# Kernel tuning notes

Measured on AMD Instinct MI355X. Metric: run time of the kernel, lower is better.

The kernel has to match this reference:

```python
import jax, jax.numpy as jnp
import numpy as np

# LLaMA-style decoder config (shrunken for reference): L layers, hidden D, H heads,
# SwiGLU width F, vocab V, LoRA rank R.
B, S, D, H, F, V, L, R = 2, 512, 1024, 16, 4096, 32000, 2, 16
DH = D // H
LORA_ALPHA = 32.0
EPS = 1e-5
ROPE_THETA = 10000.0


def setup_inputs() -> dict:
    key = jax.random.key(0)
    ks = iter(jax.random.split(key, 40))
    def n(shape, std=0.02):
        return jax.random.normal(next(ks), shape, jnp.float32) * std
    return {
        "input_ids": jax.random.randint(next(ks), (B, S), 0, V),
        "attention_mask": jnp.ones((B, S), jnp.int32),
        "embed": n((V, D)),
        "ln1": jnp.ones((L, D), jnp.float32),
        "ln2": jnp.ones((L, D), jnp.float32),
        "wq": n((L, D, D)), "aq": n((L, D, R)), "bq": n((L, R, D), 0.01),
        "wk": n((L, D, D)), "ak": n((L, D, R)), "bk": n((L, R, D), 0.01),
        "wv": n((L, D, D)), "av": n((L, D, R)), "bv": n((L, R, D), 0.01),
        "wo": n((L, D, D)), "ao": n((L, D, R)), "bo": n((L, R, D), 0.01),
        "wg": n((L, D, F)), "ag": n((L, D, R)), "bg": n((L, R, F), 0.01),
        "wu": n((L, D, F)), "au": n((L, D, R)), "bu": n((L, R, F), 0.01),
        "wd": n((L, F, D)), "ad": n((L, F, R)), "bd": n((L, R, D), 0.01),
        "final_ln": jnp.ones((D,), jnp.float32),
        "lm_head_w": n((D, V)),
        "value_w": n((D, 1)),
        "value_b": jnp.zeros((1,), jnp.float32),
    }


def _rmsnorm(x, w):
    return x * jax.lax.rsqrt(jnp.mean(x * x, axis=-1, keepdims=True) + EPS) * w


def _lin_lora(x, w, a, b):
    # base matmul + low-rank LoRA update scaled by alpha/r (dropout=eval/off)
    return x @ w + ((x @ a) @ b) * (LORA_ALPHA / R)


def _rope_cache(seq_len):
    half = DH // 2
    inv = 1.0 / (ROPE_THETA ** (jnp.arange(half, dtype=jnp.float32) / half))
    ang = jnp.arange(seq_len, dtype=jnp.float32)[:, None] * inv  # [S, half]
    ang = jnp.concatenate([ang, ang], axis=-1)                   # [S, DH]
    return jnp.cos(ang), jnp.sin(ang)


def _apply_rope(x, cos, sin):  # x: [B,S,H,DH]
    h = DH // 2
    rot = jnp.concatenate([-x[..., h:], x[..., :h]], axis=-1)
    return x * cos[None, :, None, :] + rot * sin[None, :, None, :]


def reference(input_ids, attention_mask, embed, ln1, ln2,
              wq, aq, bq, wk, ak, bk, wv, av, bv, wo, ao, bo,
              wg, ag, bg, wu, au, bu, wd, ad, bd,
              final_ln, lm_head_w, value_w, value_b):
    h = embed[input_ids]  # [B,S,D]
    cos, sin = _rope_cache(S)
    causal = jnp.tril(jnp.ones((S, S), bool))
    keep = causal[None, None, :, :] & (attention_mask[:, None, None, :] > 0)
    bias = jnp.where(keep, 0.0, -1e9)  # [B,1,S,S]
    scale = 1.0 / jnp.sqrt(jnp.float32(DH))

    for i in range(L):
        # --- self-attention block ---
        x = _rmsnorm(h, ln1[i])
        q = _lin_lora(x, wq[i], aq[i], bq[i]).reshape(B, S, H, DH)
        k = _lin_lora(x, wk[i], ak[i], bk[i]).reshape(B, S, H, DH)
        v = _lin_lora(x, wv[i], av[i], bv[i]).reshape(B, S, H, DH)
        q = _apply_rope(q, cos, sin)
        k = _apply_rope(k, cos, sin)
        scores = jnp.einsum("bqhd,bkhd->bhqk", q, k) * scale + bias
        attn = jax.nn.softmax(scores, axis=-1)
        o = jnp.einsum("bhqk,bkhd->bqhd", attn, v).reshape(B, S, D)
        h = h + _lin_lora(o, wo[i], ao[i], bo[i])
        # --- SwiGLU MLP block ---
        x = _rmsnorm(h, ln2[i])
        g = jax.nn.silu(_lin_lora(x, wg[i], ag[i], bg[i]))
        u = _lin_lora(x, wu[i], au[i], bu[i])
        h = h + _lin_lora(g * u, wd[i], ad[i], bd[i])

    h = _rmsnorm(h, final_ln)          # HF hidden_states[-1] is post final norm
    logits = h @ lm_head_w             # [B,S,V]
    values = (h @ value_w)[..., 0] + value_b[0]  # [B,S] (squeeze(-1))
    return logits, values
```

## Files before the change

kernel.cpp:

```cpp
#include <hip/hip_runtime.h>
#include <math.h>

constexpr int B = 2, S = 512, D = 1024, H = 16, F = 4096, V = 32000, L = 2, R = 16, DH = 64;
constexpr int BS = B * S;
constexpr float LORA_SCALE = 2.0f;
constexpr float EPS = 1e-5f;
constexpr int RS_QKV = 3 * D;
constexpr int RS_GU  = 2 * F;

typedef __attribute__((ext_vector_type(8))) __bf16 bf16x8;
typedef __attribute__((ext_vector_type(4))) float f32x4;

__device__ __forceinline__ unsigned short f2bf(float f) {
  unsigned u = __builtin_bit_cast(unsigned, f);
  unsigned r = (u + 0x7FFFu + ((u >> 16) & 1u)) >> 16;
  return (unsigned short)r;
}
__device__ __forceinline__ float bf2f(unsigned short us) {
  return __builtin_bit_cast(float, (unsigned)us << 16);
}
__device__ __forceinline__ void load_lds16(const void* g, void* l) {
  __builtin_amdgcn_global_load_lds((const __attribute__((address_space(1))) void*)g,
                                   (__attribute__((address_space(3))) void*)l, 16, 0, 0);
}

struct Ptr3 { const float* p[3]; };

__global__ void rope_cache_kernel(float* __restrict__ cosb, float* __restrict__ sinb) {
  int s = blockIdx.x, j = threadIdx.x;
  float inv = __expf(-(float)j * (9.210340371976184f / 32.0f));
  float ang = (float)s * inv;
  float c = cosf(ang), sn = sinf(ang);
  cosb[s * DH + j] = c;  cosb[s * DH + j + 32] = c;
  sinb[s * DH + j] = sn; sinb[s * DH + j + 32] = sn;
}

__global__ void embed_kernel(const int* __restrict__ ids, const float* __restrict__ emb,
                             float* __restrict__ h) {
  int row = blockIdx.x, t = threadIdx.x;
  int id = ids[row];
  ((float4*)(h + (size_t)row * D))[t] = ((const float4*)(emb + (size_t)id * D))[t];
}

__global__ void rmsnorm_bf16_kernel(const float* __restrict__ x, const float* __restrict__ w,
                                    unsigned short* __restrict__ y) {
  int row = blockIdx.x, t = threadIdx.x;
  float4 xv = ((const float4*)(x + (size_t)row * D))[t];
  float ss = xv.x * xv.x + xv.y * xv.y + xv.z * xv.z + xv.w * xv.w;
  __shared__ float red[256];
  red[t] = ss; __syncthreads();
  for (int s2 = 128; s2; s2 >>= 1) { if (t < s2) red[t] += red[t + s2]; __syncthreads(); }
  float rinv = rsqrtf(red[0] * (1.0f / D) + EPS);
  float4 wv = ((const float4*)w)[t];
  ushort4 o;
  o.x = f2bf(xv.x * rinv * wv.x); o.y = f2bf(xv.y * rinv * wv.y);
  o.z = f2bf(xv.z * rinv * wv.z); o.w = f2bf(xv.w * rinv * wv.w);
  ((ushort4*)(y + (size_t)row * D))[t] = o;
}

template <int NA>
__global__ void rms_lora_kernel(const float* __restrict__ hp, const float* __restrict__ w,
                                Ptr3 ap, unsigned short* __restrict__ xbf,
                                unsigned short* __restrict__ t2e) {
  int row = blockIdx.x, t = threadIdx.x;
  __shared__ float xs[D];
  __shared__ float red[256];
  float4 xv = ((const float4*)(hp + (size_t)row * D))[t];
  float ss = xv.x * xv.x + xv.y * xv.y + xv.z * xv.z + xv.w * xv.w;
  red[t] = ss; __syncthreads();
  for (int s2 = 128; s2; s2 >>= 1) { if (t < s2) red[t] += red[t + s2]; __syncthreads(); }
  float rinv = rsqrtf(red[0] * (1.0f / D) + EPS);
  float4 wv = ((const float4*)w)[t];
  float4 nx;
  nx.x = xv.x * rinv * wv.x; nx.y = xv.y * rinv * wv.y;
  nx.z = xv.z * rinv * wv.z; nx.w = xv.w * rinv * wv.w;
  xs[t * 4 + 0] = nx.x; xs[t * 4 + 1] = nx.y; xs[t * 4 + 2] = nx.z; xs[t * 4 + 3] = nx.w;
  ushort4 o;
  o.x = f2bf(nx.x); o.y = f2bf(nx.y); o.z = f2bf(nx.z); o.w = f2bf(nx.w);
  ((ushort4*)(xbf + (size_t)row * D))[t] = o;
  if (t >= NA * 16 && t < 64) t2e[(size_t)row * 64 + t] = 0;
  __syncthreads();
  int n = t & 15, g = t >> 4;
#pragma unroll
  for (int ad = 0; ad < NA; ++ad) {
    const float* a = ap.p[ad];
    float s = 0.0f;
    for (int k = g; k < D; k += 16) s = fmaf(xs[k], a[k * 16 + n], s);
    red[t] = s; __syncthreads();
    for (int h2 = 128; h2 >= 16; h2 >>= 1) { if (t < h2) red[t] += red[t + h2]; __syncthreads(); }
    if (t < 16) t2e[(size_t)row * 64 + ad * 16 + t] = f2bf(LORA_SCALE * red[t]);
    __syncthreads();
  }
}

__global__ void lora_o_kernel(const unsigned short* __restrict__ xb, const float* __restrict__ a,
                              unsigned short* __restrict__ t2e) {
  int row = blockIdx.x, t = threadIdx.x;
  __shared__ float xs[D];
  __shared__ float red[256];
  for (int k = t; k < D; k += 256) xs[k] = bf2f(xb[(size_t)row * D + k]);
  if (t >= 16 && t < 64) t2e[(size_t)row * 64 + t] = 0;
  __syncthreads();
  int n = t & 15, g = t >> 4;
  float s = 0.0f;
  for (int k = g; k < D; k += 16) s = fmaf(xs[k], a[k * 16 + n], s);
  red[t] = s; __syncthreads();
  for (int h2 = 128; h2 >= 16; h2 >>= 1) { if (t < h2) red[t] += red[t + h2]; __syncthreads(); }
  if (t < 16) t2e[(size_t)row * 64 + t] = f2bf(LORA_SCALE * red[t]);
}

__global__ void silu_lora_kernel(const unsigned short* __restrict__ gub, const float* __restrict__ a,
                                 unsigned short* __restrict__ gbf, unsigned short* __restrict__ t2e) {
  int row = blockIdx.x, t = threadIdx.x;
  __shared__ float xs[F];
  __shared__ float red[256];
#pragma unroll
  for (int i2 = 0; i2 < 2; ++i2) {
    int idx = i2 * 256 + t;
    uint4 gv = ((const uint4*)(gub + (size_t)row * RS_GU))[idx];
    uint4 uv = ((const uint4*)(gub + (size_t)row * RS_GU + F))[idx];
    const unsigned* gw = (const unsigned*)&gv;
    const unsigned* uw = (const unsigned*)&uv;
    unsigned short go[8];
#pragma unroll
    for (int q = 0; q < 4; ++q) {
      float g0 = bf2f((unsigned short)(gw[q] & 0xffff)), g1 = bf2f((unsigned short)(gw[q] >> 16));
      float u0 = bf2f((unsigned short)(uw[q] & 0xffff)), u1 = bf2f((unsigned short)(uw[q] >> 16));
      float r0 = g0 / (1.0f + __expf(-g0)) * u0;
      float r1 = g1 / (1.0f + __expf(-g1)) * u1;
      xs[idx * 8 + q * 2] = r0; xs[idx * 8 + q * 2 + 1] = r1;
      go[q * 2] = f2bf(r0); go[q * 2 + 1] = f2bf(r1);
    }
    *(uint4*)(gbf + (size_t)row * F + idx * 8) = *(const uint4*)go;
  }
  if (t >= 16 && t < 64) t2e[(size_t)row * 64 + t] = 0;
  __syncthreads();
  int n = t & 15, g = t >> 4;
  float s = 0.0f;
  for (int k = g; k < F; k += 16) s = fmaf(xs[k], a[k * 16 + n], s);
  red[t] = s; __syncthreads();
  for (int h2 = 128; h2 >= 16; h2 >>= 1) { if (t < h2) red[t] += red[t + h2]; __syncthreads(); }
  if (t < 16) t2e[(size_t)row * 64 + t] = f2bf(LORA_SCALE * red[t]);
}

struct BD { const float* p0; const float* p1; const float* p2;
            unsigned short* dst; int NA; int logW; int nelem; };
struct BDs { BD d[8]; };
__global__ void bext_many_kernel(BDs da) {
  int gid = blockIdx.x * 256 + threadIdx.x;
  int di = 0;
  while (gid >= da.d[di].nelem) { gid -= da.d[di].nelem; ++di; }
  const BD dd = da.d[di];
  int n = gid >> 6, kk = gid & 63;
  int W = 1 << dd.logW;
  int sel = n >> dd.logW;
  const float* bp = (sel == 0) ? dd.p0 : (sel == 1) ? dd.p1 : dd.p2;
  float v = 0.0f;
  if ((kk >> 4) == sel && sel < dd.NA)
    v = bp[(size_t)(kk & 15) * W + (n & (W - 1))];
  dd.dst[(size_t)n * 64 + kk] = f2bf(v);
}

struct TD { const float* src; unsigned short* dst; int K; int N; int nblk; };
struct TDs { TD d[15]; };
__global__ __launch_bounds__(256) void transpose_many_kernel(TDs da) {
  __shared__ unsigned short tile[64 * 68];
  int bid = blockIdx.x;
  int di = 0;
  while (bid >= da.d[di].nblk) { bid -= da.d[di].nblk; ++di; }
  const TD dd = da.d[di];
  int nbx = dd.N >> 6;
  int n0 = (bid % nbx) * 64, k0 = (bid / nbx) * 64;
  int t = threadIdx.x;
  int rr = t >> 4, c4 = (t & 15) << 2;
#pragma unroll
  for (int i = 0; i < 4; ++i) {
    int row = i * 16 + rr;
    float4 v = *(const float4*)(dd.src + (size_t)(k0 + row) * dd.N + n0 + c4);
    tile[(c4 + 0) * 68 + row] = f2bf(v.x);
    tile[(c4 + 1) * 68 + row] = f2bf(v.y);
    tile[(c4 + 2) * 68 + row] = f2bf(v.z);
    tile[(c4 + 3) * 68 + row] = f2bf(v.w);
  }
  __syncthreads();
#pragma unroll
  for (int i = 0; i < 4; ++i) {
    int row = i * 16 + rr;
    *(ushort4*)(dd.dst + (size_t)(n0 + row) * dd.K + k0 + c4) = *(const ushort4*)(tile + row * 68 + c4);
  }
}

template <int BN, bool ACC, bool EXT, int OM>
__global__ __launch_bounds__(256) void gemm_bf16_kernel(
    const unsigned short* __restrict__ A, const unsigned short* __restrict__ Bt,
    void* __restrict__ Cp, int M, int N, int K,
    const unsigned short* __restrict__ Ae, const unsigned short* __restrict__ Be,
    const float* __restrict__ cosb, const float* __restrict__ sinb) {
  constexpr int WM = (BN == 128) ? 2 : 4;
  constexpr int RW = 128 / WM;
  constexpr int MI = RW / 16;
  constexpr int BCH = BN / 32;
  __shared__ __align__(16) unsigned short As[2][128 * 64];
  __shared__ __align__(16) unsigned short Bs[2][BN * 64];
  int t = threadIdx.x;
  int lane = t & 63, wave = t >> 6;
  int wr = (BN == 128) ? (wave >> 1) : wave;
  int wc = (BN == 128) ? (wave & 1) : 0;
  int MT = gridDim.y, NT = gridDim.x;
  int nwg = MT * NT;
  int orig = blockIdx.y * NT + blockIdx.x;
  int qq = nwg >> 3, rr8 = nwg & 7;
  int xcd = orig & 7, pos = orig >> 3;
  int wg = (xcd < rr8) ? (xcd * (qq + 1) + pos) : (rr8 * (qq + 1) + (xcd - rr8) * qq + pos);
  int m0 = (wg % MT) * 128, n0 = (wg / MT) * BN;
  int fr = lane & 15, fq = lane >> 4;
  int xorv = fr & 7;
  f32x4 acc[MI][4] = {};
  int kIters = K / 64;
  int nIters = EXT ? kIters + 1 : kIters;

  auto STAGE = [&](int it, int buf) {
    bool ext = EXT && (it == kIters);
    int k0 = it * 64;
#pragma unroll
    for (int c = 0; c < 4; ++c) {
      int i = c * 256 + t;
      int row = i >> 3, c8 = i & 7;
      int sc = (c8 ^ (row & 7)) * 8;
      const unsigned short* src = ext ? (Ae + (size_t)(m0 + row) * 64 + sc)
                                      : (A + (size_t)(m0 + row) * K + k0 + sc);
      load_lds16(src, &As[buf][i * 8]);
    }
#pragma unroll
    for (int c = 0; c < BCH; ++c) {
      int i = c * 256 + t;
      int row = i >> 3, c8 = i & 7;
      int sc = (c8 ^ (row & 7)) * 8;
      const unsigned short* src = ext ? (Be + (size_t)(n0 + row) * 64 + sc)
                                      : (Bt + (size_t)(n0 + row) * K + k0 + sc);
      load_lds16(src, &Bs[buf][i * 8]);
    }
  };

  STAGE(0, 0);
  if (nIters > 1) STAGE(1, 1);
  int cur = 0;
  for (int it = 0; it < nIters; ++it) {
    if (it + 1 < nIters) {
      if constexpr (BN == 128) asm volatile("s_waitcnt vmcnt(8)" ::: "memory");
      else                     asm volatile("s_waitcnt vmcnt(6)" ::: "memory");
    } else {
      asm volatile("s_waitcnt vmcnt(0)" ::: "memory");
    }
    __builtin_amdgcn_s_barrier();
#pragma unroll
    for (int kk = 0; kk < 2; ++kk) {
      bf16x8 af[MI], bfr[4];
#pragma unroll
      for (int mi = 0; mi < MI; ++mi)
        af[mi] = *(const bf16x8*)(&As[cur][(wr * RW + mi * 16 + fr) * 64 + (((kk * 4 + fq) ^ xorv) << 3)]);
#pragma unroll
      for (int ni = 0; ni < 4; ++ni)
        bfr[ni] = *(const bf16x8*)(&Bs[cur][(wc * 64 + ni * 16 + fr) * 64 + (((kk * 4 + fq) ^ xorv) << 3)]);
#pragma unroll
      for (int mi = 0; mi < MI; ++mi)
#pragma unroll
        for (int ni = 0; ni < 4; ++ni)
          acc[mi][ni] = __builtin_amdgcn_mfma_f32_16x16x32_bf16(af[mi], bfr[ni], acc[mi][ni], 0, 0, 0);
    }
    __builtin_amdgcn_s_barrier();
    if (it + 2 < nIters) STAGE(it + 2, cur);
    cur ^= 1;
  }
  if constexpr (OM == 0) {
    float* C = (float*)Cp;
#pragma unroll
    for (int mi = 0; mi < MI; ++mi)
#pragma unroll
      for (int ni = 0; ni < 4; ++ni)
#pragma unroll
        for (int j = 0; j < 4; ++j) {
          int r = m0 + wr * RW + mi * 16 + fq * 4 + j;
          int cl = n0 + wc * 64 + ni * 16 + fr;
          size_t idx = (size_t)r * N + cl;
          float v = acc[mi][ni][j];
          C[idx] = ACC ? C[idx] + v : v;
        }
  } else {
    unsigned short* Cb = (unsigned short*)Cp;
#pragma unroll
    for (int mi = 0; mi < MI; ++mi)
#pragma unroll
      for (int j = 0; j < 4; ++j) {
        int r = m0 + wr * RW + mi * 16 + fq * 4 + j;
        if constexpr (OM == 2) {
          int s = r & (S - 1);
#pragma unroll
          for (int ni = 0; ni < 2; ++ni) {
            int cl0 = n0 + wc * 64 + ni * 16 + fr;
            int cl1 = cl0 + 32;
            float x0 = acc[mi][ni][j], x1 = acc[mi][ni + 2][j];
            if (cl0 < 2 * D) {
              int dh = cl0 & 63;
              float cz = cosb[s * DH + dh], sz = sinb[s * DH + dh];
              float y0 = x0 * cz - x1 * sz;
              float y1 = x1 * cz + x0 * sz;
              x0 = y0; x1 = y1;
            }
            Cb[(size_t)r * N + cl0] = f2bf(x0);
            Cb[(size_t)r * N + cl1] = f2bf(x1);
          }
        } else {
#pragma unroll
          for (int ni = 0; ni < 4; ++ni) {
            int cl = n0 + wc * 64 + ni * 16 + fr;
            Cb[(size_t)r * N + cl] = f2bf(acc[mi][ni][j]);
          }
        }
      }
  }
}

__global__ __launch_bounds__(256) void attn_mfma_kernel(
    const unsigned short* __restrict__ qkvb, const int* __restrict__ amask,
    unsigned short* __restrict__ o) {
  __shared__ unsigned short Qs[64 * 72];
  __shared__ unsigned short Ks[64 * 72];
  __shared__ unsigned short Vt[64 * 72];
  __shared__ unsigned short Ps[4][16 * 72];
  __shared__ float msk[64];
  int bid = blockIdx.x;
  int qt = bid & 7, hh = (bid >> 3) & (H - 1), b = bid >> 7;
  int t = threadIdx.x;
  int lane = t & 63, w = t >> 6;
  int fr = lane & 15, fq = lane >> 4;
  size_t rowbase = (size_t)b * S;
  int q0 = qt * 64;
  const float scale = 0.125f;
#pragma unroll
  for (int c = 0; c < 2; ++c) {
    int i = c * 256 + t;
    int row = i >> 3, ch = i & 7;
    uint4 v = *(const uint4*)(qkvb + (rowbase + q0 + row) * RS_QKV + hh * DH + ch * 8);
    *(uint4*)(Qs + row * 72 + ch * 8) = v;
  }
  f32x4 oacc[4] = {};
  float m_old[4] = {-1e30f, -1e30f, -1e30f, -1e30f};
  float l[4] = {};
  int qbase = q0 + w * 16;
  for (int kt = 0; kt <= qt; ++kt) {
    int kk0 = kt * 64;
#pragma unroll
    for (int c = 0; c < 2; ++c) {
      int i = c * 256 + t;
      int row = i >> 3, ch = i & 7;
      uint4 kv = *(const uint4*)(qkvb + (rowbase + kk0 + row) * RS_QKV + D + hh * DH + ch * 8);
      *(uint4*)(Ks + row * 72 + ch * 8) = kv;
      uint4 vv = *(const uint4*)(qkvb + (rowbase + kk0 + row) * RS_QKV + 2 * D + hh * DH + ch * 8);
      const unsigned short* vs = (const unsigned short*)&vv;
#pragma unroll
      for (int q = 0; q < 8; ++q) Vt[(ch * 8 + q) * 72 + row] = vs[q];
    }
    if (t < 64) msk[t] = (amask[b * S + kk0 + t] > 0) ? 0.0f : -1e9f;
    __syncthreads();
    bf16x8 aq[2];
    aq[0] = *(const bf16x8*)(Qs + (w * 16 + fr) * 72 + fq * 8);
    aq[1] = *(const bf16x8*)(Qs + (w * 16 + fr) * 72 + 32 + fq * 8);
    f32x4 sacc[4];
#pragma unroll
    for (int ct = 0; ct < 4; ++ct) {
      bf16x8 bk0 = *(const bf16x8*)(Ks + (ct * 16 + fr) * 72 + fq * 8);
      bf16x8 bk1 = *(const bf16x8*)(Ks + (ct * 16 + fr) * 72 + 32 + fq * 8);
      f32x4 z = {};
      z = __builtin_amdgcn_mfma_f32_16x16x32_bf16(aq[0], bk0, z, 0, 0, 0);
      sacc[ct] = __builtin_amdgcn_mfma_f32_16x16x32_bf16(aq[1], bk1, z, 0, 0, 0);
    }
    float sv[4][4];
#pragma unroll
    for (int ct = 0; ct < 4; ++ct) {
      int kg = kk0 + ct * 16 + fr;
      float mk = msk[ct * 16 + fr];
#pragma unroll
      for (int j = 0; j < 4; ++j) {
        int qg = qbase + fq * 4 + j;
        float s = sacc[ct][j] * scale + mk;
        sv[ct][j] = (kg > qg) ? -1e9f : s;
      }
    }
    float mnew[4], f[4], rsum[4];
#pragma unroll
    for (int j = 0; j < 4; ++j) {
      float mt = fmaxf(fmaxf(sv[0][j], sv[1][j]), fmaxf(sv[2][j], sv[3][j]));
      for (int off = 1; off < 16; off <<= 1) mt = fmaxf(mt, __shfl_xor(mt, off));
      mnew[j] = fmaxf(m_old[j], mt);
      f[j] = __expf(m_old[j] - mnew[j]);
      float rs = 0.0f;
#pragma unroll
      for (int ct = 0; ct < 4; ++ct) {
        float e = __expf(sv[ct][j] - mnew[j]);
        sv[ct][j] = e;
        rs += e;
      }
      for (int off = 1; off < 16; off <<= 1) rs += __shfl_xor(rs, off);
      rsum[j] = rs;
      l[j] = l[j] * f[j] + rsum[j];
      m_old[j] = mnew[j];
#pragma unroll
      for (int dt = 0; dt < 4; ++dt) oacc[dt][j] *= f[j];
    }
#pragma unroll
    for (int ct = 0; ct < 4; ++ct)
#pragma unroll
      for (int j = 0; j < 4; ++j)
        Ps[w][(fq * 4 + j) * 72 + ct * 16 + fr] = f2bf(sv[ct][j]);
    __syncthreads();
    bf16x8 pa[2];
    pa[0] = *(const bf16x8*)(&Ps[w][fr * 72 + fq * 8]);
    pa[1] = *(const bf16x8*)(&Ps[w][fr * 72 + 32 + fq * 8]);
#pragma unroll
    for (int dt = 0; dt < 4; ++dt) {
      bf16x8 vb0 = *(const bf16x8*)(Vt + (dt * 16 + fr) * 72 + fq * 8);
      bf16x8 vb1 = *(const bf16x8*)(Vt + (dt * 16 + fr) * 72 + 32 + fq * 8);
      oacc[dt] = __builtin_amdgcn_mfma_f32_16x16x32_bf16(pa[0], vb0, oacc[dt], 0, 0, 0);
      oacc[dt] = __builtin_amdgcn_mfma_f32_16x16x32_bf16(pa[1], vb1, oacc[dt], 0, 0, 0);
    }
    __syncthreads();
  }
#pragma unroll
  for (int j = 0; j < 4; ++j) {
    float rinv = 1.0f / l[j];
    int qrow = qbase + fq * 4 + j;
#pragma unroll
    for (int dt = 0; dt < 4; ++dt)
      o[(rowbase + qrow) * D + hh * DH + dt * 16 + fr] = f2bf(oacc[dt][j] * rinv);
  }
}

__global__ void value_kernel(const unsigned short* __restrict__ hf, const float* __restrict__ vw,
                             const float* __restrict__ vb, float* __restrict__ out) {
  int row = blockIdx.x, t = threadIdx.x;
  float acc = 0.0f;
  for (int d = t; d < D; d += 256) acc = fmaf(bf2f(hf[(size_t)row * D + d]), vw[d], acc);
  __shared__ float red[256];
  red[t] = acc; __syncthreads();
  for (int s2 = 128; s2; s2 >>= 1) { if (t < s2) red[t] += red[t + s2]; __syncthreads(); }
  if (t == 0) out[row] = red[0] + vb[0];
}

extern "C" void kernel_launch(void* const* d_in, const int* in_sizes, int n_in,
                              void* d_out, int out_size, void* d_ws, size_t ws_size,
                              hipStream_t stream) {
  const int*   ids     = (const int*)d_in[0];
  const int*   amask   = (const int*)d_in[1];
  const float* emb     = (const float*)d_in[2];
  const float* ln1     = (const float*)d_in[3];
  const float* ln2     = (const float*)d_in[4];
  const float* wq = (const float*)d_in[5],  *aq = (const float*)d_in[6],  *bq = (const float*)d_in[7];
  const float* wk = (const float*)d_in[8],  *ak = (const float*)d_in[9],  *bk = (const float*)d_in[10];
  const float* wv = (const float*)d_in[11], *av = (const float*)d_in[12], *bv = (const float*)d_in[13];
  const float* wo = (const float*)d_in[14], *ao = (const float*)d_in[15], *bo = (const float*)d_in[16];
  const float* wg = (const float*)d_in[17], *ag = (const float*)d_in[18], *bg = (const float*)d_in[19];
  const float* wu = (const float*)d_in[20], *au = (const float*)d_in[21], *bu = (const float*)d_in[22];
  const float* wd = (const float*)d_in[23], *ad = (const float*)d_in[24], *bd = (const float*)d_in[25];
  const float* final_ln  = (const float*)d_in[26];
  const float* lm_head_w = (const float*)d_in[27];
  const float* value_w   = (const float*)d_in[28];
  const float* value_b   = (const float*)d_in[29];

  float* out    = (float*)d_out;
  float* logits = out;
  float* values = out + (size_t)BS * V;

  float* Wf = (float*)d_ws;
  float* cosb = Wf; Wf += S * DH;
  float* sinb = Wf; Wf += S * DH;
  float* h    = Wf; Wf += (size_t)BS * D;
  unsigned short* Wb = (unsigned short*)Wf;
  unsigned short* x_bf  = Wb; Wb += (size_t)BS * D;
  unsigned short* t2e   = Wb; Wb += (size_t)BS * 64;
  unsigned short* qg    = Wb; Wb += (size_t)BS * F;
  unsigned short* gu_bf = Wb; Wb += (size_t)BS * RS_GU;
  unsigned short* wqkvT = Wb; Wb += (size_t)L * 3 * D * D;
  unsigned short* woT   = Wb; Wb += (size_t)L * D * D;
  unsigned short* wguT  = Wb; Wb += (size_t)L * 2 * D * F;
  unsigned short* wdT   = Wb; Wb += (size_t)L * F * D;
  unsigned short* lmT   = Wb; Wb += (size_t)D * V;
  unsigned short* beQKV = Wb; Wb += (size_t)L * 3 * D * 64;
  unsigned short* beO   = Wb; Wb += (size_t)L * D * 64;
  unsigned short* beGU  = Wb; Wb += (size_t)L * 2 * F * 64;
  unsigned short* beD   = Wb; Wb += (size_t)L * D * 64;
  unsigned short* qkv_bf = qg;
  unsigned short* gbf    = qg;
  unsigned short* obf    = gu_bf;

  TDs td; int tblocks = 0; int di = 0;
  auto addT = [&](const float* s, unsigned short* dp, int K_, int N_) {
    td.d[di] = {s, dp, K_, N_, (K_ / 64) * (N_ / 64)};
    tblocks += td.d[di].nblk; ++di;
  };
  for (int l = 0; l < L; ++l) {
    size_t DD = (size_t)D * D, DF = (size_t)D * F;
    addT(wq + l * DD, wqkvT + (size_t)l * 3 * DD, D, D);
    addT(wk + l * DD, wqkvT + (size_t)l * 3 * DD + DD, D, D);
    addT(wv + l * DD, wqkvT + (size_t)l * 3 * DD + 2 * DD, D, D);
    addT(wo + l * DD, woT + l * DD, D, D);
    addT(wg + l * DF, wguT + (size_t)l * 2 * DF, D, F);
    addT(wu + l * DF, wguT + (size_t)l * 2 * DF + DF, D, F);
    addT(wd + l * DF, wdT + l * DF, F, D);
  }
  addT(lm_head_w, lmT, D, V);
  transpose_many_kernel<<<dim3(tblocks), 256, 0, stream>>>(td);

  BDs bd2; int belems = 0; di = 0;
  auto addB = [&](const float* p0, const float* p1, const float* p2,
                  unsigned short* dst, int NA, int logW, int N_) {
    bd2.d[di] = {p0, p1, p2, dst, NA, logW, N_ * 64};
    belems += N_ * 64; ++di;
  };
  for (int l = 0; l < L; ++l) {
    size_t oRD = (size_t)l * R * D, oRF = (size_t)l * R * F;
    addB(bq + oRD, bk + oRD, bv + oRD, beQKV + (size_t)l * 3 * D * 64, 3, 10, 3 * D);
    addB(bo + oRD, nullptr, nullptr,   beO   + (size_t)l * D * 64,     1, 10, D);
    addB(bg + oRF, bu + oRF, nullptr,  beGU  + (size_t)l * 2 * F * 64, 2, 12, 2 * F);
    addB(bd + oRD, nullptr, nullptr,   beD   + (size_t)l * D * 64,     1, 10, D);
  }
  bext_many_kernel<<<dim3(belems / 256), 256, 0, stream>>>(bd2);

  rope_cache_kernel<<<dim3(S), dim3(32), 0, stream>>>(cosb, sinb);
  embed_kernel<<<dim3(BS), dim3(256), 0, stream>>>(ids, emb, h);

  for (int l = 0; l < L; ++l) {
    size_t DD = (size_t)D * D, DF = (size_t)D * F;
    size_t oDR = (size_t)l * D * R, oFR = (size_t)l * F * R;

    { Ptr3 ap = {{aq + oDR, ak + oDR, av + oDR}};
      rms_lora_kernel<3><<<dim3(BS), 256, 0, stream>>>(h, ln1 + (size_t)l * D, ap, x_bf, t2e); }
    gemm_bf16_kernel<128, false, true, 2><<<dim3(3 * D / 128, BS / 128), 256, 0, stream>>>(
        x_bf, wqkvT + (size_t)l * 3 * DD, qkv_bf, BS, 3 * D, D,
        t2e, beQKV + (size_t)l * 3 * D * 64, cosb, sinb);

    attn_mfma_kernel<<<dim3(B * H * (S / 64)), 256, 0, stream>>>(qkv_bf, amask, obf);

    lora_o_kernel<<<dim3(BS), 256, 0, stream>>>(obf, ao + oDR, t2e);
    gemm_bf16_kernel<64, true, true, 0><<<dim3(D / 64, BS / 128), 256, 0, stream>>>(
        obf, woT + l * DD, h, BS, D, D, t2e, beO + (size_t)l * D * 64, nullptr, nullptr);

    { Ptr3 ap = {{ag + oDR, au + oDR, nullptr}};
      rms_lora_kernel<2><<<dim3(BS), 256, 0, stream>>>(h, ln2 + (size_t)l * D, ap, x_bf, t2e); }
    gemm_bf16_kernel<128, false, true, 1><<<dim3(2 * F / 128, BS / 128), 256, 0, stream>>>(
        x_bf, wguT + (size_t)l * 2 * DF, gu_bf, BS, 2 * F, D,
        t2e, beGU + (size_t)l * 2 * F * 64, nullptr, nullptr);

    silu_lora_kernel<<<dim3(BS), 256, 0, stream>>>(gu_bf, ad + oFR, gbf, t2e);

    gemm_bf16_kernel<64, true, true, 0><<<dim3(D / 64, BS / 128), 256, 0, stream>>>(
        gbf, wdT + l * DF, h, BS, D, F, t2e, beD + (size_t)l * D * 64, nullptr, nullptr);
  }

  rmsnorm_bf16_kernel<<<dim3(BS), 256, 0, stream>>>(h, final_ln, x_bf);
  gemm_bf16_kernel<128, false, false, 0><<<dim3(V / 128, BS / 128), 256, 0, stream>>>(
      x_bf, lmT, logits, BS, V, D, nullptr, nullptr, nullptr, nullptr);
  value_kernel<<<dim3(BS), 256, 0, stream>>>(x_bf, value_w, value_b, values);
}
```

Measured before the change: 1.022 ms.

## Shuffle-based LoRA reductions, wider swizzled transpose, smaller attention tiles, MFMA priority hints

Replaces the shared-memory tree reductions in the LoRA projection kernels with wave shuffles plus a four-way LDS combine, cutting barriers. The weight transpose now handles 128x64 tiles with an XOR-swizzled LDS layout and fully coalesced 128-element row writes, halving block count. Attention is split into 32-query tiles with 128-thread blocks, doubling the grid and trimming causal work per block. s_setprio hints are wrapped around the MFMA loops in GEMM and attention to favour matrix issue.

```diff
diff --git a/kernel.cpp b/kernel.cpp
--- a/kernel.cpp
+++ b/kernel.cpp
@@ -63,6 +63,7 @@
                                 Ptr3 ap, unsigned short* __restrict__ xbf,
                                 unsigned short* __restrict__ t2e) {
   int row = blockIdx.x, t = threadIdx.x;
+  int lane = t & 63;
   __shared__ float xs[D];
   __shared__ float red[256];
   float4 xv = ((const float4*)(hp + (size_t)row * D))[t];
@@ -86,34 +87,42 @@
     const float* a = ap.p[ad];
     float s = 0.0f;
     for (int k = g; k < D; k += 16) s = fmaf(xs[k], a[k * 16 + n], s);
-    red[t] = s; __syncthreads();
-    for (int h2 = 128; h2 >= 16; h2 >>= 1) { if (t < h2) red[t] += red[t + h2]; __syncthreads(); }
-    if (t < 16) t2e[(size_t)row * 64 + ad * 16 + t] = f2bf(LORA_SCALE * red[t]);
+    s += __shfl_xor(s, 16);
+    s += __shfl_xor(s, 32);
+    if (lane < 16) red[(t >> 6) * 16 + n] = s;
     __syncthreads();
+    if (t < 16) t2e[(size_t)row * 64 + ad * 16 + t] =
+        f2bf(LORA_SCALE * (red[t] + red[t + 16] + red[t + 32] + red[t + 48]));
+    if (ad + 1 < NA) __syncthreads();
   }
 }
 
 __global__ void lora_o_kernel(const unsigned short* __restrict__ xb, const float* __restrict__ a,
                               unsigned short* __restrict__ t2e) {
   int row = blockIdx.x, t = threadIdx.x;
+  int lane = t & 63;
   __shared__ float xs[D];
-  __shared__ float red[256];
+  __shared__ float red[64];
   for (int k = t; k < D; k += 256) xs[k] = bf2f(xb[(size_t)row * D + k]);
   if (t >= 16 && t < 64) t2e[(size_t)row * 64 + t] = 0;
   __syncthreads();
   int n = t & 15, g = t >> 4;
   float s = 0.0f;
   for (int k = g; k < D; k += 16) s = fmaf(xs[k], a[k * 16 + n], s);
-  red[t] = s; __syncthreads();
-  for (int h2 = 128; h2 >= 16; h2 >>= 1) { if (t < h2) red[t] += red[t + h2]; __syncthreads(); }
-  if (t < 16) t2e[(size_t)row * 64 + t] = f2bf(LORA_SCALE * red[t]);
+  s += __shfl_xor(s, 16);
+  s += __shfl_xor(s, 32);
+  if (lane < 16) red[(t >> 6) * 16 + n] = s;
+  __syncthreads();
+  if (t < 16) t2e[(size_t)row * 64 + t] =
+      f2bf(LORA_SCALE * (red[t] + red[t + 16] + red[t + 32] + red[t + 48]));
 }
 
 __global__ void silu_lora_kernel(const unsigned short* __restrict__ gub, const float* __restrict__ a,
                                  unsigned short* __restrict__ gbf, unsigned short* __restrict__ t2e) {
   int row = blockIdx.x, t = threadIdx.x;
+  int lane = t & 63;
   __shared__ float xs[F];
-  __shared__ float red[256];
+  __shared__ float red[64];
 #pragma unroll
   for (int i2 = 0; i2 < 2; ++i2) {
     int idx = i2 * 256 + t;
@@ -138,9 +147,12 @@
   int n = t & 15, g = t >> 4;
   float s = 0.0f;
   for (int k = g; k < F; k += 16) s = fmaf(xs[k], a[k * 16 + n], s);
-  red[t] = s; __syncthreads();
-  for (int h2 = 128; h2 >= 16; h2 >>= 1) { if (t < h2) red[t] += red[t + h2]; __syncthreads(); }
-  if (t < 16) t2e[(size_t)row * 64 + t] = f2bf(LORA_SCALE * red[t]);
+  s += __shfl_xor(s, 16);
+  s += __shfl_xor(s, 32);
+  if (lane < 16) red[(t >> 6) * 16 + n] = s;
+  __syncthreads();
+  if (t < 16) t2e[(size_t)row * 64 + t] =
+      f2bf(LORA_SCALE * (red[t] + red[t + 16] + red[t + 32] + red[t + 48]));
 }
 
 struct BD { const float* p0; const float* p1; const float* p2;
@@ -164,29 +176,32 @@
 struct TD { const float* src; unsigned short* dst; int K; int N; int nblk; };
 struct TDs { TD d[15]; };
 __global__ __launch_bounds__(256) void transpose_many_kernel(TDs da) {
-  __shared__ unsigned short tile[64 * 68];
+  __shared__ unsigned short tile[64 * 136];
   int bid = blockIdx.x;
   int di = 0;
   while (bid >= da.d[di].nblk) { bid -= da.d[di].nblk; ++di; }
   const TD dd = da.d[di];
   int nbx = dd.N >> 6;
-  int n0 = (bid % nbx) * 64, k0 = (bid / nbx) * 64;
+  int n0 = (bid % nbx) * 64, k0 = (bid / nbx) * 128;
   int t = threadIdx.x;
   int rr = t >> 4, c4 = (t & 15) << 2;
 #pragma unroll
-  for (int i = 0; i < 4; ++i) {
+  for (int i = 0; i < 8; ++i) {
     int row = i * 16 + rr;
     float4 v = *(const float4*)(dd.src + (size_t)(k0 + row) * dd.N + n0 + c4);
-    tile[(c4 + 0) * 68 + row] = f2bf(v.x);
-    tile[(c4 + 1) * 68 + row] = f2bf(v.y);
-    tile[(c4 + 2) * 68 + row] = f2bf(v.z);
-    tile[(c4 + 3) * 68 + row] = f2bf(v.w);
+    tile[(c4 + 0) * 136 + (row ^ ((((c4 + 0) >> 2) & 7) << 2))] = f2bf(v.x);
+    tile[(c4 + 1) * 136 + (row ^ ((((c4 + 1) >> 2) & 7) << 2))] = f2bf(v.y);
+    tile[(c4 + 2) * 136 + (row ^ ((((c4 + 2) >> 2) & 7) << 2))] = f2bf(v.z);
+    tile[(c4 + 3) * 136 + (row ^ ((((c4 + 3) >> 2) & 7) << 2))] = f2bf(v.w);
   }
   __syncthreads();
 #pragma unroll
-  for (int i = 0; i < 4; ++i) {
-    int row = i * 16 + rr;
-    *(ushort4*)(dd.dst + (size_t)(n0 + row) * dd.K + k0 + c4) = *(const ushort4*)(tile + row * 68 + c4);
+  for (int i = 0; i < 8; ++i) {
+    int flat = i * 256 + t;
+    int n = flat >> 5, cw = flat & 31;
+    int kb = (cw * 4) ^ (((n >> 2) & 7) << 2);
+    *(ushort4*)(dd.dst + (size_t)(n0 + n) * dd.K + k0 + cw * 4) =
+        *(const ushort4*)(tile + n * 136 + kb);
   }
 }
 
@@ -253,6 +268,7 @@
       asm volatile("s_waitcnt vmcnt(0)" ::: "memory");
     }
     __builtin_amdgcn_s_barrier();
+    __builtin_amdgcn_s_setprio(1);
 #pragma unroll
     for (int kk = 0; kk < 2; ++kk) {
       bf16x8 af[MI], bfr[4];
@@ -268,6 +284,7 @@
         for (int ni = 0; ni < 4; ++ni)
           acc[mi][ni] = __builtin_amdgcn_mfma_f32_16x16x32_bf16(af[mi], bfr[ni], acc[mi][ni], 0, 0, 0);
     }
+    __builtin_amdgcn_s_setprio(0);
     __builtin_amdgcn_s_barrier();
     if (it + 2 < nIters) STAGE(it + 2, cur);
     cur ^= 1;
@@ -321,38 +338,39 @@
   }
 }
 
-__global__ __launch_bounds__(256) void attn_mfma_kernel(
+__global__ __launch_bounds__(128) void attn_mfma_kernel(
     const unsigned short* __restrict__ qkvb, const int* __restrict__ amask,
     unsigned short* __restrict__ o) {
-  __shared__ unsigned short Qs[64 * 72];
+  __shared__ unsigned short Qs[32 * 72];
   __shared__ unsigned short Ks[64 * 72];
   __shared__ unsigned short Vt[64 * 72];
-  __shared__ unsigned short Ps[4][16 * 72];
+  __shared__ unsigned short Ps[2][16 * 72];
   __shared__ float msk[64];
   int bid = blockIdx.x;
-  int qt = bid & 7, hh = (bid >> 3) & (H - 1), b = bid >> 7;
+  int qt = bid & 15, hh = (bid >> 4) & (H - 1), b = bid >> 8;
   int t = threadIdx.x;
   int lane = t & 63, w = t >> 6;
   int fr = lane & 15, fq = lane >> 4;
   size_t rowbase = (size_t)b * S;
-  int q0 = qt * 64;
+  int q0 = qt * 32;
   const float scale = 0.125f;
 #pragma unroll
   for (int c = 0; c < 2; ++c) {
-    int i = c * 256 + t;
+    int i = c * 128 + t;
     int row = i >> 3, ch = i & 7;
-    uint4 v = *(const uint4*)(qkvb + (rowbase + q0 + row) * RS_QKV + hh * DH + ch * 8);
-    *(uint4*)(Qs + row * 72 + ch * 8) = v;
+    *(uint4*)(Qs + row * 72 + ch * 8) =
+        *(const uint4*)(qkvb + (rowbase + q0 + row) * RS_QKV + hh * DH + ch * 8);
   }
   f32x4 oacc[4] = {};
   float m_old[4] = {-1e30f, -1e30f, -1e30f, -1e30f};
   float l[4] = {};
   int qbase = q0 + w * 16;
-  for (int kt = 0; kt <= qt; ++kt) {
+  int nkt = ((q0 + 31) >> 6) + 1;
+  for (int kt = 0; kt < nkt; ++kt) {
     int kk0 = kt * 64;
 #pragma unroll
-    for (int c = 0; c < 2; ++c) {
-      int i = c * 256 + t;
+    for (int c = 0; c < 4; ++c) {
+      int i = c * 128 + t;
       int row = i >> 3, ch = i & 7;
       uint4 kv = *(const uint4*)(qkvb + (rowbase + kk0 + row) * RS_QKV + D + hh * DH + ch * 8);
       *(uint4*)(Ks + row * 72 + ch * 8) = kv;
@@ -367,6 +385,7 @@
     aq[0] = *(const bf16x8*)(Qs + (w * 16 + fr) * 72 + fq * 8);
     aq[1] = *(const bf16x8*)(Qs + (w * 16 + fr) * 72 + 32 + fq * 8);
     f32x4 sacc[4];
+    __builtin_amdgcn_s_setprio(1);
 #pragma unroll
     for (int ct = 0; ct < 4; ++ct) {
       bf16x8 bk0 = *(const bf16x8*)(Ks + (ct * 16 + fr) * 72 + fq * 8);
@@ -375,6 +394,7 @@
       z = __builtin_amdgcn_mfma_f32_16x16x32_bf16(aq[0], bk0, z, 0, 0, 0);
       sacc[ct] = __builtin_amdgcn_mfma_f32_16x16x32_bf16(aq[1], bk1, z, 0, 0, 0);
     }
+    __builtin_amdgcn_s_setprio(0);
     float sv[4][4];
 #pragma unroll
     for (int ct = 0; ct < 4; ++ct) {
@@ -417,6 +437,7 @@
     bf16x8 pa[2];
     pa[0] = *(const bf16x8*)(&Ps[w][fr * 72 + fq * 8]);
     pa[1] = *(const bf16x8*)(&Ps[w][fr * 72 + 32 + fq * 8]);
+    __builtin_amdgcn_s_setprio(1);
 #pragma unroll
     for (int dt = 0; dt < 4; ++dt) {
       bf16x8 vb0 = *(const bf16x8*)(Vt + (dt * 16 + fr) * 72 + fq * 8);
@@ -424,6 +445,7 @@
       oacc[dt] = __builtin_amdgcn_mfma_f32_16x16x32_bf16(pa[0], vb0, oacc[dt], 0, 0, 0);
       oacc[dt] = __builtin_amdgcn_mfma_f32_16x16x32_bf16(pa[1], vb1, oacc[dt], 0, 0, 0);
     }
+    __builtin_amdgcn_s_setprio(0);
     __syncthreads();
   }
 #pragma unroll
@@ -495,7 +517,7 @@
 
   TDs td; int tblocks = 0; int di = 0;
   auto addT = [&](const float* s, unsigned short* dp, int K_, int N_) {
-    td.d[di] = {s, dp, K_, N_, (K_ / 64) * (N_ / 64)};
+    td.d[di] = {s, dp, K_, N_, (K_ / 128) * (N_ / 64)};
     tblocks += td.d[di].nblk; ++di;
   };
   for (int l = 0; l < L; ++l) {
@@ -539,7 +561,7 @@
         x_bf, wqkvT + (size_t)l * 3 * DD, qkv_bf, BS, 3 * D, D,
         t2e, beQKV + (size_t)l * 3 * D * 64, cosb, sinb);
 
-    attn_mfma_kernel<<<dim3(B * H * (S / 64)), 256, 0, stream>>>(qkv_bf, amask, obf);
+    attn_mfma_kernel<<<dim3(B * H * (S / 32)), 128, 0, stream>>>(qkv_bf, amask, obf);
 
     lora_o_kernel<<<dim3(BS), 256, 0, stream>>>(obf, ao + oDR, t2e);
     gemm_bf16_kernel<64, true, true, 0><<<dim3(D / 64, BS / 128), 256, 0, stream>>>(
```

New measurement: 1.045 ms. +2.2%, slower.
